# Kernel optimization log

Measured on AMD Instinct MI355X. Metric: run time of the kernel, lower is better.

The kernel has to match this reference:

```python
import jax, jax.numpy as jnp
import numpy as np

BSZ, L, D_INNER, D_STATE = 2, 2048, 2048, 8
DT_RANK = D_INNER // 8  # 256


def setup_inputs() -> dict:
    key = jax.random.key(0)
    k0, k1, k2, k3 = jax.random.split(key, 4)
    x = jax.random.normal(k0, (BSZ, L, D_INNER), jnp.float32)
    # x_proj: Linear(d_inner -> dt_rank + 2*d_state), no bias
    W_xproj = jax.random.normal(k1, (DT_RANK + 2 * D_STATE, D_INNER), jnp.float32) * 0.02
    # dt_proj: Linear(dt_rank -> d_inner), uniform(-dt_rank^-0.5, +)
    std = DT_RANK ** -0.5
    W_dt = jax.random.uniform(k2, (D_INNER, DT_RANK), jnp.float32, -std, std)
    # dt bias init: inverse-softplus of dt ~ LogUniform(1e-3, 1e-1)
    dt = jnp.exp(jax.random.uniform(k3, (D_INNER,), jnp.float32)
                 * (jnp.log(0.1) - jnp.log(0.001)) + jnp.log(0.001))
    dt = jnp.clip(dt, 1e-4)
    b_dt = dt + jnp.log(-jnp.expm1(-dt))
    # A = repeat(arange(1, N+1), 'n -> d n'); A_log = log(A)
    A_log = jnp.log(jnp.broadcast_to(
        jnp.arange(1, D_STATE + 1, dtype=jnp.float32), (D_INNER, D_STATE)))
    D_param = jnp.ones((D_INNER,), jnp.float32)
    return {"x": x, "W_xproj": W_xproj, "W_dt": W_dt, "b_dt": b_dt,
            "A_log": A_log, "D_param": D_param}


def reference(x, W_xproj, W_dt, b_dt, A_log, D_param):
    # x: (B, L, D)
    d_state = A_log.shape[1]
    dt_rank = W_dt.shape[1]
    x_dbl = jnp.einsum('bld,kd->blk', x, W_xproj)          # (B,L,dt_rank+2N)
    dt_r = x_dbl[..., :dt_rank]
    B_ssm = x_dbl[..., dt_rank:dt_rank + d_state]          # (B,L,N)
    C_ssm = x_dbl[..., dt_rank + d_state:]                 # (B,L,N)
    delta = jax.nn.softplus(jnp.einsum('blr,dr->bld', dt_r, W_dt) + b_dt)  # (B,L,D) > 0
    A = -jnp.exp(A_log)                                     # (D,N) < 0
    # Discretization: dA = exp(delta*A), dBu = delta*B*u
    dA = jnp.exp(delta[..., None] * A)                      # (B,L,D,N)
    dBu = (delta * x)[..., None] * B_ssm[:, :, None, :]     # (B,L,D,N)

    # Linear recurrence h_t = dA_t * h_{t-1} + dBu_t via associative scan over L
    def combine(c1, c2):
        a1, b1 = c1
        a2, b2 = c2
        return a1 * a2, a2 * b1 + b2

    _, h = jax.lax.associative_scan(combine, (dA, dBu), axis=1)  # (B,L,D,N)
    y = jnp.einsum('bldn,bln->bld', h, C_ssm) + x * D_param
    return y
```

## Files before the change

### kernel.cpp

```cpp
#include <hip/hip_runtime.h>
#include <math.h>

#define BSZ    2
#define LSEQ   2048
#define DI     2048
#define DSTATE 8
#define DTRANK 256
#define KXP    (DTRANK + 2 * DSTATE)
#define NPAD   288
#define NC     64
#define CL     (LSEQ / NC)
#define KSPLIT 8
#define KCHUNK (DI / KSPLIT)

#define NWXP (288u * 2048u)
#define NWX  (272u * 2048u)
#define NWDT (2048u * 256u)

typedef __attribute__((ext_vector_type(8))) short bf16x8;
typedef __attribute__((ext_vector_type(4))) float f32x4;

static __device__ __forceinline__ unsigned short f2bf(float f) {
    unsigned u = __float_as_uint(f);
    u += 0x7fff + ((u >> 16) & 1);
    return (unsigned short)(u >> 16);
}
static __device__ __forceinline__ float bf2f(unsigned short s) {
    return __uint_as_float((unsigned)s << 16);
}

static __device__ __forceinline__ float softplus_fast(float z) {
    const float e = __expf(-fabsf(z));
    return fmaxf(z, 0.0f) + __logf(1.0f + e);
}

__global__ __launch_bounds__(256) void convert_w(const float* __restrict__ Wx,
                                                 const float* __restrict__ Wdt,
                                                 unsigned short* __restrict__ Wxb,
                                                 unsigned short* __restrict__ Wdtb) {
    const unsigned tid = blockIdx.x * 256 + threadIdx.x;
    const unsigned i4 = tid * 4;
    float4 v;
    unsigned short* dst;
    unsigned j;
    if (i4 < NWXP) {
        j = i4;
        v = (j < NWX) ? *(const float4*)&Wx[j] : make_float4(0.f, 0.f, 0.f, 0.f);
        dst = Wxb;
    } else {
        j = i4 - NWXP;
        if (j >= NWDT) return;
        v = *(const float4*)&Wdt[j];
        dst = Wdtb;
    }
    ushort4 o;
    o.x = f2bf(v.x); o.y = f2bf(v.y); o.z = f2bf(v.z); o.w = f2bf(v.w);
    *(ushort4*)&dst[j] = o;
}

#define G1RS 40
__global__ __launch_bounds__(256) void gemm1_mfma(const float* __restrict__ x,
                                                  const unsigned short* __restrict__ Wxb,
                                                  unsigned short* __restrict__ partb) {
    __shared__ __align__(16) unsigned short As[64 * G1RS];
    __shared__ __align__(16) unsigned short Bs[288 * G1RS];
    const int mt   = blockIdx.x;
    const int ks   = blockIdx.y;
    const int t    = threadIdx.x;
    const int wave = t >> 6;
    const int lane = t & 63;
    const int quad = lane >> 4;
    const int r    = lane & 15;
    const int rh   = wave >> 1;
    const int nh   = wave & 1;
    const int m0   = mt * 64;

    const int arow = t >> 2;
    const int aoff = (t & 3) * 8;

    f32x4 acc[2][9];
#pragma unroll
    for (int f = 0; f < 2; f++)
#pragma unroll
        for (int n = 0; n < 9; n++) acc[f][n] = (f32x4)(0.0f);

    const int kbeg = ks * KCHUNK;
    for (int k0 = kbeg; k0 < kbeg + KCHUNK; k0 += 32) {
        const float4 a0 = *(const float4*)&x[(size_t)(m0 + arow) * DI + k0 + aoff];
        const float4 a1 = *(const float4*)&x[(size_t)(m0 + arow) * DI + k0 + aoff + 4];
        bf16x8 bstage[5];
#pragma unroll
        for (int j = 0; j < 5; j++) {
            const int i = t + j * 256;
            if (i < 1152)
                bstage[j] = *(const bf16x8*)&Wxb[(size_t)(i >> 2) * DI + k0 + (i & 3) * 8];
        }
        __syncthreads();
        bf16x8 av;
        av[0] = (short)f2bf(a0.x); av[1] = (short)f2bf(a0.y);
        av[2] = (short)f2bf(a0.z); av[3] = (short)f2bf(a0.w);
        av[4] = (short)f2bf(a1.x); av[5] = (short)f2bf(a1.y);
        av[6] = (short)f2bf(a1.z); av[7] = (short)f2bf(a1.w);
        *(bf16x8*)&As[arow * G1RS + aoff] = av;
#pragma unroll
        for (int j = 0; j < 5; j++) {
            const int i = t + j * 256;
            if (i < 1152)
                *(bf16x8*)&Bs[(i >> 2) * G1RS + (i & 3) * 8] = bstage[j];
        }
        __syncthreads();

        bf16x8 af[2], bf[9];
#pragma unroll
        for (int f = 0; f < 2; f++)
            af[f] = *(const bf16x8*)&As[(rh * 32 + f * 16 + r) * G1RS + quad * 8];
#pragma unroll
        for (int nf = 0; nf < 9; nf++)
            bf[nf] = *(const bf16x8*)&Bs[(nh * 144 + nf * 16 + r) * G1RS + quad * 8];
#pragma unroll
        for (int f = 0; f < 2; f++)
#pragma unroll
            for (int nf = 0; nf < 9; nf++)
                acc[f][nf] = __builtin_amdgcn_mfma_f32_16x16x32_bf16(af[f], bf[nf], acc[f][nf], 0, 0, 0);
    }

    unsigned short* p = partb + (size_t)ks * 4096 * NPAD;
#pragma unroll
    for (int f = 0; f < 2; f++) {
        const int row0 = m0 + rh * 32 + f * 16 + quad * 4;
#pragma unroll
        for (int nf = 0; nf < 9; nf++) {
            const int col = nh * 144 + nf * 16 + r;
#pragma unroll
            for (int i = 0; i < 4; i++)
                p[(size_t)(row0 + i) * NPAD + col] = f2bf(acc[f][nf][i]);
        }
    }
}

__global__ __launch_bounds__(256) void reduce1(const unsigned short* __restrict__ partb,
                                               unsigned short* __restrict__ dtr,
                                               float* __restrict__ BC) {
    const int tid = blockIdx.x * 256 + threadIdx.x;
    const int row = tid / 72;
    const int c4  = (tid - row * 72) * 4;
    float4 s = make_float4(0.f, 0.f, 0.f, 0.f);
#pragma unroll
    for (int ks = 0; ks < KSPLIT; ks++) {
        const ushort4 v = *(const ushort4*)&partb[(size_t)ks * 4096 * NPAD + (size_t)row * NPAD + c4];
        s.x += bf2f(v.x); s.y += bf2f(v.y); s.z += bf2f(v.z); s.w += bf2f(v.w);
    }
    if (c4 < DTRANK) {
        ushort4 o;
        o.x = f2bf(s.x); o.y = f2bf(s.y); o.z = f2bf(s.z); o.w = f2bf(s.w);
        *(ushort4*)&dtr[(size_t)row * DTRANK + c4] = o;
    } else if (c4 < KXP) {
        *(float4*)&BC[(size_t)row * 16 + (c4 - DTRANK)] = s;
    }
}

#define G2RS 40
__global__ __launch_bounds__(256, 2) void gemm2_mfma(const unsigned short* __restrict__ dtr,
                                                     const unsigned short* __restrict__ Wdtb,
                                                     const float* __restrict__ bdt,
                                                     unsigned short* __restrict__ deltab) {
    __shared__ __align__(16) unsigned short As[128 * G2RS];
    __shared__ __align__(16) unsigned short Bs[128 * G2RS];
    const int nt   = blockIdx.x;
    const int mt   = blockIdx.y;
    const int t    = threadIdx.x;
    const int wave = t >> 6;
    const int lane = t & 63;
    const int quad = lane >> 4;
    const int r    = lane & 15;
    const int m0 = mt * 128, n0 = nt * 128;
    const int mw = (wave >> 1) * 64, nw = (wave & 1) * 64;

    const int srow = t >> 1;
    const int sc   = (t & 1) * 16;

    f32x4 acc[4][4];
#pragma unroll
    for (int f = 0; f < 4; f++)
#pragma unroll
        for (int g = 0; g < 4; g++) acc[f][g] = (f32x4)(0.0f);

    for (int k0 = 0; k0 < DTRANK; k0 += 32) {
        const bf16x8 a0 = *(const bf16x8*)&dtr[(size_t)(m0 + srow) * DTRANK + k0 + sc];
        const bf16x8 a1 = *(const bf16x8*)&dtr[(size_t)(m0 + srow) * DTRANK + k0 + sc + 8];
        const bf16x8 b0 = *(const bf16x8*)&Wdtb[(size_t)(n0 + srow) * DTRANK + k0 + sc];
        const bf16x8 b1 = *(const bf16x8*)&Wdtb[(size_t)(n0 + srow) * DTRANK + k0 + sc + 8];
        __syncthreads();
        *(bf16x8*)&As[srow * G2RS + sc]     = a0;
        *(bf16x8*)&As[srow * G2RS + sc + 8] = a1;
        *(bf16x8*)&Bs[srow * G2RS + sc]     = b0;
        *(bf16x8*)&Bs[srow * G2RS + sc + 8] = b1;
        __syncthreads();

        bf16x8 a[4], b[4];
#pragma unroll
        for (int f = 0; f < 4; f++)
            a[f] = *(const bf16x8*)&As[(mw + f * 16 + r) * G2RS + quad * 8];
#pragma unroll
        for (int g = 0; g < 4; g++)
            b[g] = *(const bf16x8*)&Bs[(nw + g * 16 + r) * G2RS + quad * 8];
#pragma unroll
        for (int f = 0; f < 4; f++)
#pragma unroll
            for (int g = 0; g < 4; g++)
                acc[f][g] = __builtin_amdgcn_mfma_f32_16x16x32_bf16(a[f], b[g], acc[f][g], 0, 0, 0);
    }

#pragma unroll
    for (int f = 0; f < 4; f++) {
        const int row0 = m0 + mw + f * 16 + quad * 4;
#pragma unroll
        for (int g = 0; g < 4; g++) {
            const int col = n0 + nw + g * 16 + r;
            const float bv = bdt[col];
#pragma unroll
            for (int i = 0; i < 4; i++)
                deltab[(size_t)(row0 + i) * DI + col] = f2bf(softplus_fast(acc[f][g][i] + bv));
        }
    }
}

__global__ __launch_bounds__(256) void scan_pass1(const float* __restrict__ x,
                                                  const unsigned short* __restrict__ deltab,
                                                  const float* __restrict__ BC,
                                                  const float* __restrict__ Alog,
                                                  float* __restrict__ Pb,
                                                  float* __restrict__ Hb) {
    __shared__ __align__(16) float Ls[CL * 16];
    const int bi   = blockIdx.x;
    const int b    = bi >> 9;
    const int c    = (bi >> 3) & 63;
    const int dblk = bi & 7;
    const int tid  = threadIdx.x;
    const int d    = dblk * 256 + tid;
    const int l0   = c * CL;
    const size_t row0 = (size_t)b * LSEQ + l0;

    if (tid < CL * 4) {
        const int l = tid >> 2, part = (tid & 3) * 4;
        *(float4*)&Ls[l * 16 + part] = *(const float4*)&BC[(row0 + l) * 16 + part];
    }

    float A[8], P[8], H[8];
#pragma unroll
    for (int n = 0; n < 8; n++) {
        A[n] = -__expf(Alog[d * 8 + n]);
        P[n] = 1.f;
        H[n] = 0.f;
    }
    __syncthreads();

#pragma unroll 4
    for (int l = 0; l < CL; l++) {
        const size_t row = row0 + l;
        const float dl = bf2f(deltab[row * DI + d]);
        const float xv = x[row * DI + d];
        const float du = dl * xv;
#pragma unroll
        for (int n = 0; n < 8; n++) {
            const float dA = __expf(dl * A[n]);
            H[n] = dA * H[n] + du * Ls[l * 16 + n];
            P[n] *= dA;
        }
    }
    const size_t base = ((size_t)(b * NC + c) * DI + d) * 8;
    *(float4*)&Pb[base]     = make_float4(P[0], P[1], P[2], P[3]);
    *(float4*)&Pb[base + 4] = make_float4(P[4], P[5], P[6], P[7]);
    *(float4*)&Hb[base]     = make_float4(H[0], H[1], H[2], H[3]);
    *(float4*)&Hb[base + 4] = make_float4(H[4], H[5], H[6], H[7]);
}

__global__ __launch_bounds__(256) void scan_pass2(const float* __restrict__ Pb,
                                                  const float* __restrict__ Hb,
                                                  float* __restrict__ h0) {
    const int t   = blockIdx.x * 256 + threadIdx.x;
    const int b   = t >> 14;
    const int rem = t & 16383;
    float h = 0.f;
#pragma unroll 4
    for (int c = 0; c < NC; c++) {
        const size_t base = (size_t)(b * NC + c) * (DI * 8) + rem;
        h0[base] = h;
        h = Pb[base] * h + Hb[base];
    }
}

__global__ __launch_bounds__(256) void scan_pass3(const float* __restrict__ x,
                                                  const unsigned short* __restrict__ deltab,
                                                  const float* __restrict__ BC,
                                                  const float* __restrict__ Alog,
                                                  const float* __restrict__ Dp,
                                                  const float* __restrict__ h0,
                                                  float* __restrict__ y) {
    __shared__ __align__(16) float Ls[CL * 16];
    const int bi   = blockIdx.x;
    const int b    = bi >> 9;
    const int c    = (bi >> 3) & 63;
    const int dblk = bi & 7;
    const int tid  = threadIdx.x;
    const int d    = dblk * 256 + tid;
    const int l0   = c * CL;
    const size_t row0 = (size_t)b * LSEQ + l0;

    if (tid < CL * 4) {
        const int l = tid >> 2, part = (tid & 3) * 4;
        *(float4*)&Ls[l * 16 + part] = *(const float4*)&BC[(row0 + l) * 16 + part];
    }

    float A[8], h[8];
    const size_t hbase = ((size_t)(b * NC + c) * DI + d) * 8;
    const float4 h0a = *(const float4*)&h0[hbase];
    const float4 h0b = *(const float4*)&h0[hbase + 4];
    h[0] = h0a.x; h[1] = h0a.y; h[2] = h0a.z; h[3] = h0a.w;
    h[4] = h0b.x; h[5] = h0b.y; h[6] = h0b.z; h[7] = h0b.w;
#pragma unroll
    for (int n = 0; n < 8; n++) A[n] = -__expf(Alog[d * 8 + n]);
    const float Dpar = Dp[d];
    __syncthreads();

#pragma unroll 4
    for (int l = 0; l < CL; l++) {
        const size_t row = row0 + l;
        const float dl = bf2f(deltab[row * DI + d]);
        const float xv = x[row * DI + d];
        const float du = dl * xv;
        float yv = 0.f;
#pragma unroll
        for (int n = 0; n < 8; n++) {
            const float dA = __expf(dl * A[n]);
            h[n] = dA * h[n] + du * Ls[l * 16 + n];
            yv += h[n] * Ls[l * 16 + 8 + n];
        }
        y[row * DI + d] = yv + xv * Dpar;
    }
}

extern "C" void kernel_launch(void* const* d_in, const int* in_sizes, int n_in,
                              void* d_out, int out_size, void* d_ws, size_t ws_size,
                              hipStream_t stream) {
    const float* x    = (const float*)d_in[0];
    const float* Wx   = (const float*)d_in[1];
    const float* Wdt  = (const float*)d_in[2];
    const float* bdt  = (const float*)d_in[3];
    const float* Alog = (const float*)d_in[4];
    const float* Dp   = (const float*)d_in[5];
    float* y = (float*)d_out;

    float* ws = (float*)d_ws;
    unsigned short* partb  = (unsigned short*)ws;
    unsigned short* deltab = (unsigned short*)ws;
    float* BC = ws + 4718592;
    float* Pb = ws + 4784128;
    float* Hb = ws + 6881280;
    float* h0 = ws + 8978432;
    unsigned short* Wxb  = (unsigned short*)(ws + 11075584);
    unsigned short* Wdtb = (unsigned short*)(ws + 11370496);
    unsigned short* dtr  = (unsigned short*)(ws + 11632640);

    dim3 blk(256);
    hipLaunchKernelGGL(convert_w, dim3((NWXP + NWDT) / 4 / 256), blk, 0, stream,
                       Wx, Wdt, Wxb, Wdtb);
    hipLaunchKernelGGL(gemm1_mfma, dim3(64, KSPLIT), blk, 0, stream, x, Wxb, partb);
    hipLaunchKernelGGL(reduce1, dim3(4096 * 72 / 256), blk, 0, stream, partb, dtr, BC);
    hipLaunchKernelGGL(gemm2_mfma, dim3(16, 32), blk, 0, stream, dtr, Wdtb, bdt, deltab);
    hipLaunchKernelGGL(scan_pass1, dim3(BSZ * NC * 8), blk, 0, stream, x, deltab, BC, Alog, Pb, Hb);
    hipLaunchKernelGGL(scan_pass2, dim3(128), blk, 0, stream, Pb, Hb, h0);
    hipLaunchKernelGGL(scan_pass3, dim3(BSZ * NC * 8), blk, 0, stream, x, deltab, BC, Alog, Dp, h0, y);
}
```

Before: 189.0 us.

## Fuse weight bf16 conversion into GEMMs and emit bf16 x for scan passes

```diff
diff --git a/kernel.cpp b/kernel.cpp
--- a/kernel.cpp
+++ b/kernel.cpp
@@ -13,10 +13,6 @@
 #define KSPLIT 8
 #define KCHUNK (DI / KSPLIT)
 
-#define NWXP (288u * 2048u)
-#define NWX  (272u * 2048u)
-#define NWDT (2048u * 256u)
-
 typedef __attribute__((ext_vector_type(8))) short bf16x8;
 typedef __attribute__((ext_vector_type(4))) float f32x4;
 
@@ -34,34 +30,11 @@
     return fmaxf(z, 0.0f) + __logf(1.0f + e);
 }
 
-__global__ __launch_bounds__(256) void convert_w(const float* __restrict__ Wx,
-                                                 const float* __restrict__ Wdt,
-                                                 unsigned short* __restrict__ Wxb,
-                                                 unsigned short* __restrict__ Wdtb) {
-    const unsigned tid = blockIdx.x * 256 + threadIdx.x;
-    const unsigned i4 = tid * 4;
-    float4 v;
-    unsigned short* dst;
-    unsigned j;
-    if (i4 < NWXP) {
-        j = i4;
-        v = (j < NWX) ? *(const float4*)&Wx[j] : make_float4(0.f, 0.f, 0.f, 0.f);
-        dst = Wxb;
-    } else {
-        j = i4 - NWXP;
-        if (j >= NWDT) return;
-        v = *(const float4*)&Wdt[j];
-        dst = Wdtb;
-    }
-    ushort4 o;
-    o.x = f2bf(v.x); o.y = f2bf(v.y); o.z = f2bf(v.z); o.w = f2bf(v.w);
-    *(ushort4*)&dst[j] = o;
-}
-
 #define G1RS 40
 __global__ __launch_bounds__(256) void gemm1_mfma(const float* __restrict__ x,
-                                                  const unsigned short* __restrict__ Wxb,
-                                                  unsigned short* __restrict__ partb) {
+                                                  const float* __restrict__ Wx,
+                                                  unsigned short* __restrict__ partb,
+                                                  unsigned short* __restrict__ xb) {
     __shared__ __align__(16) unsigned short As[64 * G1RS];
     __shared__ __align__(16) unsigned short Bs[288 * G1RS];
     const int mt   = blockIdx.x;
@@ -92,8 +65,20 @@
 #pragma unroll
         for (int j = 0; j < 5; j++) {
             const int i = t + j * 256;
-            if (i < 1152)
-                bstage[j] = *(const bf16x8*)&Wxb[(size_t)(i >> 2) * DI + k0 + (i & 3) * 8];
+            if (i < 1152) {
+                const int row = i >> 2, koff = (i & 3) * 8;
+                float4 u0 = make_float4(0.f, 0.f, 0.f, 0.f), u1 = u0;
+                if (row < KXP) {
+                    u0 = *(const float4*)&Wx[(size_t)row * DI + k0 + koff];
+                    u1 = *(const float4*)&Wx[(size_t)row * DI + k0 + koff + 4];
+                }
+                bf16x8 bv;
+                bv[0] = (short)f2bf(u0.x); bv[1] = (short)f2bf(u0.y);
+                bv[2] = (short)f2bf(u0.z); bv[3] = (short)f2bf(u0.w);
+                bv[4] = (short)f2bf(u1.x); bv[5] = (short)f2bf(u1.y);
+                bv[6] = (short)f2bf(u1.z); bv[7] = (short)f2bf(u1.w);
+                bstage[j] = bv;
+            }
         }
         __syncthreads();
         bf16x8 av;
@@ -102,6 +87,7 @@
         av[4] = (short)f2bf(a1.x); av[5] = (short)f2bf(a1.y);
         av[6] = (short)f2bf(a1.z); av[7] = (short)f2bf(a1.w);
         *(bf16x8*)&As[arow * G1RS + aoff] = av;
+        *(bf16x8*)&xb[(size_t)(m0 + arow) * DI + k0 + aoff] = av;
 #pragma unroll
         for (int j = 0; j < 5; j++) {
             const int i = t + j * 256;
@@ -110,18 +96,18 @@
         }
         __syncthreads();
 
-        bf16x8 af[2], bf[9];
+        bf16x8 af[2], bfv[9];
 #pragma unroll
         for (int f = 0; f < 2; f++)
             af[f] = *(const bf16x8*)&As[(rh * 32 + f * 16 + r) * G1RS + quad * 8];
 #pragma unroll
         for (int nf = 0; nf < 9; nf++)
-            bf[nf] = *(const bf16x8*)&Bs[(nh * 144 + nf * 16 + r) * G1RS + quad * 8];
+            bfv[nf] = *(const bf16x8*)&Bs[(nh * 144 + nf * 16 + r) * G1RS + quad * 8];
 #pragma unroll
         for (int f = 0; f < 2; f++)
 #pragma unroll
             for (int nf = 0; nf < 9; nf++)
-                acc[f][nf] = __builtin_amdgcn_mfma_f32_16x16x32_bf16(af[f], bf[nf], acc[f][nf], 0, 0, 0);
+                acc[f][nf] = __builtin_amdgcn_mfma_f32_16x16x32_bf16(af[f], bfv[nf], acc[f][nf], 0, 0, 0);
     }
 
     unsigned short* p = partb + (size_t)ks * 4096 * NPAD;
@@ -161,7 +147,7 @@
 
 #define G2RS 40
 __global__ __launch_bounds__(256, 2) void gemm2_mfma(const unsigned short* __restrict__ dtr,
-                                                     const unsigned short* __restrict__ Wdtb,
+                                                     const float* __restrict__ Wdt,
                                                      const float* __restrict__ bdt,
                                                      unsigned short* __restrict__ deltab) {
     __shared__ __align__(16) unsigned short As[128 * G2RS];
@@ -188,11 +174,22 @@
     for (int k0 = 0; k0 < DTRANK; k0 += 32) {
         const bf16x8 a0 = *(const bf16x8*)&dtr[(size_t)(m0 + srow) * DTRANK + k0 + sc];
         const bf16x8 a1 = *(const bf16x8*)&dtr[(size_t)(m0 + srow) * DTRANK + k0 + sc + 8];
-        const bf16x8 b0 = *(const bf16x8*)&Wdtb[(size_t)(n0 + srow) * DTRANK + k0 + sc];
-        const bf16x8 b1 = *(const bf16x8*)&Wdtb[(size_t)(n0 + srow) * DTRANK + k0 + sc + 8];
+        const float4 w0 = *(const float4*)&Wdt[(size_t)(n0 + srow) * DTRANK + k0 + sc];
+        const float4 w1 = *(const float4*)&Wdt[(size_t)(n0 + srow) * DTRANK + k0 + sc + 4];
+        const float4 w2 = *(const float4*)&Wdt[(size_t)(n0 + srow) * DTRANK + k0 + sc + 8];
+        const float4 w3 = *(const float4*)&Wdt[(size_t)(n0 + srow) * DTRANK + k0 + sc + 12];
         __syncthreads();
         *(bf16x8*)&As[srow * G2RS + sc]     = a0;
         *(bf16x8*)&As[srow * G2RS + sc + 8] = a1;
+        bf16x8 b0, b1;
+        b0[0] = (short)f2bf(w0.x); b0[1] = (short)f2bf(w0.y);
+        b0[2] = (short)f2bf(w0.z); b0[3] = (short)f2bf(w0.w);
+        b0[4] = (short)f2bf(w1.x); b0[5] = (short)f2bf(w1.y);
+        b0[6] = (short)f2bf(w1.z); b0[7] = (short)f2bf(w1.w);
+        b1[0] = (short)f2bf(w2.x); b1[1] = (short)f2bf(w2.y);
+        b1[2] = (short)f2bf(w2.z); b1[3] = (short)f2bf(w2.w);
+        b1[4] = (short)f2bf(w3.x); b1[5] = (short)f2bf(w3.y);
+        b1[6] = (short)f2bf(w3.z); b1[7] = (short)f2bf(w3.w);
         *(bf16x8*)&Bs[srow * G2RS + sc]     = b0;
         *(bf16x8*)&Bs[srow * G2RS + sc + 8] = b1;
         __syncthreads();
@@ -225,7 +222,7 @@
     }
 }
 
-__global__ __launch_bounds__(256) void scan_pass1(const float* __restrict__ x,
+__global__ __launch_bounds__(256) void scan_pass1(const unsigned short* __restrict__ xb,
                                                   const unsigned short* __restrict__ deltab,
                                                   const float* __restrict__ BC,
                                                   const float* __restrict__ Alog,
@@ -255,11 +252,11 @@
     }
     __syncthreads();
 
-#pragma unroll 4
+#pragma unroll 8
     for (int l = 0; l < CL; l++) {
         const size_t row = row0 + l;
         const float dl = bf2f(deltab[row * DI + d]);
-        const float xv = x[row * DI + d];
+        const float xv = bf2f(xb[row * DI + d]);
         const float du = dl * xv;
 #pragma unroll
         for (int n = 0; n < 8; n++) {
@@ -275,14 +272,14 @@
     *(float4*)&Hb[base + 4] = make_float4(H[4], H[5], H[6], H[7]);
 }
 
-__global__ __launch_bounds__(256) void scan_pass2(const float* __restrict__ Pb,
-                                                  const float* __restrict__ Hb,
-                                                  float* __restrict__ h0) {
-    const int t   = blockIdx.x * 256 + threadIdx.x;
+__global__ __launch_bounds__(64) void scan_pass2(const float* __restrict__ Pb,
+                                                 const float* __restrict__ Hb,
+                                                 float* __restrict__ h0) {
+    const int t   = blockIdx.x * 64 + threadIdx.x;
     const int b   = t >> 14;
     const int rem = t & 16383;
     float h = 0.f;
-#pragma unroll 4
+#pragma unroll 8
     for (int c = 0; c < NC; c++) {
         const size_t base = (size_t)(b * NC + c) * (DI * 8) + rem;
         h0[base] = h;
@@ -290,7 +287,7 @@
     }
 }
 
-__global__ __launch_bounds__(256) void scan_pass3(const float* __restrict__ x,
+__global__ __launch_bounds__(256) void scan_pass3(const unsigned short* __restrict__ xb,
                                                   const unsigned short* __restrict__ deltab,
                                                   const float* __restrict__ BC,
                                                   const float* __restrict__ Alog,
@@ -323,11 +320,11 @@
     const float Dpar = Dp[d];
     __syncthreads();
 
-#pragma unroll 4
+#pragma unroll 8
     for (int l = 0; l < CL; l++) {
         const size_t row = row0 + l;
         const float dl = bf2f(deltab[row * DI + d]);
-        const float xv = x[row * DI + d];
+        const float xv = bf2f(xb[row * DI + d]);
         const float du = dl * xv;
         float yv = 0.f;
 #pragma unroll
@@ -358,17 +355,14 @@
     float* Pb = ws + 4784128;
     float* Hb = ws + 6881280;
     float* h0 = ws + 8978432;
-    unsigned short* Wxb  = (unsigned short*)(ws + 11075584);
-    unsigned short* Wdtb = (unsigned short*)(ws + 11370496);
-    unsigned short* dtr  = (unsigned short*)(ws + 11632640);
+    unsigned short* xb  = (unsigned short*)(ws + 11075584);
+    unsigned short* dtr = (unsigned short*)(ws + 15269888);
 
     dim3 blk(256);
-    hipLaunchKernelGGL(convert_w, dim3((NWXP + NWDT) / 4 / 256), blk, 0, stream,
-                       Wx, Wdt, Wxb, Wdtb);
-    hipLaunchKernelGGL(gemm1_mfma, dim3(64, KSPLIT), blk, 0, stream, x, Wxb, partb);
+    hipLaunchKernelGGL(gemm1_mfma, dim3(64, KSPLIT), blk, 0, stream, x, Wx, partb, xb);
     hipLaunchKernelGGL(reduce1, dim3(4096 * 72 / 256), blk, 0, stream, partb, dtr, BC);
-    hipLaunchKernelGGL(gemm2_mfma, dim3(16, 32), blk, 0, stream, dtr, Wdtb, bdt, deltab);
-    hipLaunchKernelGGL(scan_pass1, dim3(BSZ * NC * 8), blk, 0, stream, x, deltab, BC, Alog, Pb, Hb);
-    hipLaunchKernelGGL(scan_pass2, dim3(128), blk, 0, stream, Pb, Hb, h0);
-    hipLaunchKernelGGL(scan_pass3, dim3(BSZ * NC * 8), blk, 0, stream, x, deltab, BC, Alog, Dp, h0, y);
-}
+    hipLaunchKernelGGL(gemm2_mfma, dim3(16, 32), blk, 0, stream, dtr, Wdt, bdt, deltab);
+    hipLaunchKernelGGL(scan_pass1, dim3(BSZ * NC * 8), blk, 0, stream, xb, deltab, BC, Alog, Pb, Hb);
+    hipLaunchKernelGGL(scan_pass2, dim3(512), dim3(64), 0, stream, Pb, Hb, h0);
+    hipLaunchKernelGGL(scan_pass3, dim3(BSZ * NC * 8), blk, 0, stream, xb, deltab, BC, Alog, Dp, h0, y);
+}
```

Measured after the change: 191.9 us. No clear change (+1.5%).
